# Performance work log

Hardware: AMD Instinct MI355X
Metric: run time of the kernel (lower is better)

The kernel has to match this reference:

```python
import jax, jax.numpy as jnp
import numpy as np

B, T, HID = 2, 2048, 2048
H, KVH, D = 16, 4, 128


def _rope_tables(t, d):
    inv_freq = 1.0 / (10000.0 ** (np.arange(0, d, 2, dtype=np.float32) / d))
    freqs = np.arange(t, dtype=np.float32)[:, None] * inv_freq[None, :]  # [T, d/2]
    emb = np.concatenate([freqs, freqs], axis=-1)  # [T, d]
    return jnp.asarray(np.cos(emb))[None], jnp.asarray(np.sin(emb))[None]  # [1,T,d]


def setup_inputs() -> dict:
    key = jax.random.key(0)
    ks = jax.random.split(key, 5)
    x = jax.random.normal(ks[0], (B, T, HID), dtype=jnp.float32)
    rope_cos, rope_sin = _rope_tables(T, D)
    s_in = 1.0 / np.sqrt(HID)
    Wq = jax.random.normal(ks[1], (HID, H * D), dtype=jnp.float32) * s_in
    Wk = jax.random.normal(ks[2], (HID, KVH * D), dtype=jnp.float32) * s_in
    Wv = jax.random.normal(ks[3], (HID, KVH * D), dtype=jnp.float32) * s_in
    Wo = jax.random.normal(ks[4], (H * D, HID), dtype=jnp.float32) * (1.0 / np.sqrt(H * D))
    return {"x": x, "rope_cos": rope_cos, "rope_sin": rope_sin,
            "Wq": Wq, "Wk": Wk, "Wv": Wv, "Wo": Wo}


def _apply_rope(t, cos, sin):
    # t: [B,T,h,D]; cos/sin: [1,T,D] -> broadcast over heads
    c = cos[:, :, None, :]
    s = sin[:, :, None, :]
    t1, t2 = jnp.split(t, 2, axis=-1)
    rot = jnp.concatenate([-t2, t1], axis=-1)
    return t * c + rot * s


def reference(x, rope_cos, rope_sin, Wq, Wk, Wv, Wo):
    Tq = x.shape[1]
    q = (x @ Wq).reshape(B, Tq, H, D)
    k = (x @ Wk).reshape(B, Tq, KVH, D)
    v = (x @ Wv).reshape(B, Tq, KVH, D)
    q = _apply_rope(q, rope_cos[:, :Tq], rope_sin[:, :Tq])
    k = _apply_rope(k, rope_cos[:, :Tq], rope_sin[:, :Tq])
    # sliding_window == T -> T <= W branch: k/v unchanged
    rep = H // KVH  # GQA repeat-kv
    k_full = jnp.repeat(k, rep, axis=2)  # [B,T,H,D]
    v_full = jnp.repeat(v, rep, axis=2)
    scale = 1.0 / jnp.sqrt(jnp.asarray(D, dtype=x.dtype))
    scores = jnp.einsum('bqhd,bkhd->bhqk', q, k_full) * scale
    causal = jnp.tril(jnp.ones((Tq, Tq), dtype=bool))  # end-aligned, Tk==Tq
    scores = jnp.where(causal[None, None], scores, jnp.asarray(-jnp.inf, scores.dtype))
    p = jax.nn.softmax(scores, axis=-1)
    out = jnp.einsum('bhqk,bkhd->bqhd', p, v_full)
    return out.reshape(B, Tq, H * D) @ Wo
```

## Files before the change

### kernel.cpp

```cpp
#include <hip/hip_runtime.h>
#include <hip/hip_bf16.h>

#define B_   2
#define T_   2048
#define HID_ 2048
#define H_   16
#define KVH_ 4
#define D_   128
#define GQ_  (H_ / KVH_)

#define QN_  8388608
#define KN_  2097152
#define TOTQ_ 4194304
#define TOTK_ 1048576

typedef unsigned short u16;
typedef __attribute__((ext_vector_type(8))) unsigned short us8v;
typedef __attribute__((ext_vector_type(8))) short s16x8;
typedef __attribute__((ext_vector_type(4))) float f32x4;

__device__ __forceinline__ float bf2f(u16 u) {
  return __uint_as_float(((unsigned)u) << 16);
}
__device__ __forceinline__ u16 f2bf(float f) {
  unsigned x = __float_as_uint(f);
  return (u16)((x + 0x7fffu + ((x >> 16) & 1u)) >> 16);
}

__device__ __forceinline__ void gl2lds(const void* gp, void* lp) {
  __builtin_amdgcn_global_load_lds(
      (const __attribute__((address_space(1))) unsigned int*)gp,
      (__attribute__((address_space(3))) unsigned int*)lp, 16, 0, 0);
}

__device__ __forceinline__ void probe2(const void* A, const void* W, int tid,
                                       bool* abf, bool* wbf) {
  __shared__ int cA, zA, cW, zW;
  if (tid == 0) { cA = 0; zA = 0; cW = 0; zW = 0; }
  __syncthreads();
  const int i = 16384 + tid;
  {
    const u16 raw = ((const u16*)A)[i];
    const float v = bf2f(raw);
    const bool bad = !(fabsf(v) <= 1e6f) ||
                     (v != 0.0f && fabsf(v) < 1e-10f);
    if (bad) atomicAdd(&cA, 1);
    if (((tid & 1) == 0) && raw == 0) atomicAdd(&zA, 1);
  }
  {
    const u16 raw = ((const u16*)W)[i];
    const float v = bf2f(raw);
    const bool bad = !(fabsf(v) <= 1e6f) ||
                     (v != 0.0f && fabsf(v) < 1e-10f);
    if (bad) atomicAdd(&cW, 1);
    if (((tid & 1) == 0) && raw == 0) atomicAdd(&zW, 1);
  }
  __syncthreads();
  *abf = (cA < 8) && (zA < 100);
  *wbf = (cW < 8) && (zW < 100);
}

__device__ void transp_body(const void* __restrict__ Wv_,
                            u16* __restrict__ WT, int K, int N, int bx,
                            int by, int tid) {
  bool wbf, dummy;
  probe2(Wv_, Wv_, tid, &wbf, &dummy);

  __shared__ float tile[64][65];
  const int kb = by * 64;
  const int nb = bx * 64;

  for (int it = tid; it < 512; it += 256) {
    const int r = it >> 3;
    const int g = it & 7;
    const size_t off = (size_t)(kb + r) * N + nb + g * 8;
    float f[8];
    if (wbf) {
      const us8v t8 = *(const us8v*)((const u16*)Wv_ + off);
#pragma unroll
      for (int e = 0; e < 8; ++e) f[e] = bf2f(t8[e]);
    } else {
      const float4 f0 = *(const float4*)((const float*)Wv_ + off);
      const float4 f1 = *(const float4*)((const float*)Wv_ + off + 4);
      f[0] = f0.x; f[1] = f0.y; f[2] = f0.z; f[3] = f0.w;
      f[4] = f1.x; f[5] = f1.y; f[6] = f1.z; f[7] = f1.w;
    }
#pragma unroll
    for (int e = 0; e < 8; ++e) tile[r][g * 8 + e] = f[e];
  }
  __syncthreads();
  for (int it = tid; it < 512; it += 256) {
    const int n = it >> 3;
    const int g = it & 7;
    us8v tmp;
#pragma unroll
    for (int e = 0; e < 8; ++e) tmp[e] = f2bf(tile[g * 8 + e][n]);
    *(us8v*)&WT[(size_t)(nb + n) * K + kb + g * 8] = tmp;
  }
}

__device__ void conv_body(const void* __restrict__ in, u16* __restrict__ outb,
                          int cb, int tid) {
  bool ibf, dummy;
  probe2(in, in, tid, &ibf, &dummy);
  const int idx = cb * 256 + tid;
  if (idx >= (QN_ / 8)) return;
  if (ibf) {
    *(us8v*)&outb[(size_t)idx * 8] =
        *(const us8v*)((const u16*)in + (size_t)idx * 8);
  } else {
    const float4 f0 = *(const float4*)((const float*)in + (size_t)idx * 8);
    const float4 f1 = *(const float4*)((const float*)in + (size_t)idx * 8 + 4);
    uint4 w;
    asm("v_cvt_pk_bf16_f32 %0, %1, %2" : "=v"(w.x) : "v"(f0.x), "v"(f0.y));
    asm("v_cvt_pk_bf16_f32 %0, %1, %2" : "=v"(w.y) : "v"(f0.z), "v"(f0.w));
    asm("v_cvt_pk_bf16_f32 %0, %1, %2" : "=v"(w.z) : "v"(f1.x), "v"(f1.y));
    asm("v_cvt_pk_bf16_f32 %0, %1, %2" : "=v"(w.w) : "v"(f1.z), "v"(f1.w));
    *(uint4*)&outb[(size_t)idx * 8] = w;
  }
}

__global__ __launch_bounds__(256) void prep_k(
    const void* __restrict__ Wq, const void* __restrict__ Wk,
    const void* __restrict__ Wv, const void* __restrict__ Wo,
    const void* __restrict__ x, u16* __restrict__ WqT,
    u16* __restrict__ WkT, u16* __restrict__ WvT, u16* __restrict__ WoT,
    u16* __restrict__ xb) {
  const int b = blockIdx.x;
  const int tid = threadIdx.x;
  if (b < 1024) {
    transp_body(Wq, WqT, HID_, H_ * D_, b & 31, b >> 5, tid);
  } else if (b < 1280) {
    const int bb = b - 1024;
    transp_body(Wk, WkT, HID_, KVH_ * D_, bb & 7, bb >> 3, tid);
  } else if (b < 1536) {
    const int bb = b - 1280;
    transp_body(Wv, WvT, HID_, KVH_ * D_, bb & 7, bb >> 3, tid);
  } else if (b < 2560) {
    const int bb = b - 1536;
    transp_body(Wo, WoT, H_ * D_, HID_, bb & 31, bb >> 5, tid);
  } else {
    conv_body(x, xb, b - 2560, tid);
  }
}

template <int OMODE, int BN>
__global__ __launch_bounds__(512, 4) void gemm_mfma(
    const u16* __restrict__ Ab, const u16* __restrict__ WT,
    void* __restrict__ Cv, int M, int N, int K) {
  const int tid = threadIdx.x;

  __shared__ __align__(16) u16 Alds[2][128 * 64];
  __shared__ __align__(16) u16 Blds[2][BN * 64];

  const int m0 = blockIdx.y * 128;
  const int n0 = blockIdx.x * BN;
  const int wave = tid >> 6;
  const int lane = tid & 63;
  const int wm = (wave >> 2) * 64;
  const int wn = (wave & 3) * (BN / 4);
  const int lrow = lane & 15;
  const int lq = lane >> 4;
  constexpr int NI = BN / 64;

  f32x4 acc[4][NI] = {};

#define G_STAGE64(bi, kk)                                                     \
  do {                                                                        \
    _Pragma("unroll") for (int _p = 0; _p < 2; ++_p) {                        \
      const int _it = tid + _p * 512;                                         \
      const int _r = _it >> 3, _g = _it & 7;                                  \
      const int _gs = _g ^ (_r & 7);                                          \
      gl2lds(Ab + (size_t)(m0 + _r) * K + (kk) + _gs * 8,                     \
             &Alds[bi][((tid & ~63) + _p * 512) * 8]);                        \
    }                                                                         \
    _Pragma("unroll") for (int _p = 0; _p < (BN / 64); ++_p) {                \
      const int _it = tid + _p * 512;                                         \
      const int _n = _it >> 3, _g = _it & 7;                                  \
      const int _gs = _g ^ (_n & 7);                                          \
      gl2lds(WT + (size_t)(n0 + _n) * K + (kk) + _gs * 8,                     \
             &Blds[bi][((tid & ~63) + _p * 512) * 8]);                        \
    }                                                                         \
  } while (0)

  G_STAGE64(0, 0);
  __syncthreads();

  int cur = 0;
  for (int k0 = 0; k0 < K; k0 += 64) {
    if (k0 + 64 < K) G_STAGE64(cur ^ 1, k0 + 64);

#pragma unroll
    for (int ks = 0; ks < 2; ++ks) {
      s16x8 af[4], bfr[NI];
#pragma unroll
      for (int mi = 0; mi < 4; ++mi) {
        const int row = wm + 16 * mi + lrow;
        af[mi] = *(const s16x8*)&Alds[cur][row * 64 +
                                           (((ks * 4 + lq) ^ (row & 7)) * 8)];
      }
#pragma unroll
      for (int ni = 0; ni < NI; ++ni) {
        const int row = wn + 16 * ni + lrow;
        bfr[ni] = *(const s16x8*)&Blds[cur][row * 64 +
                                            (((ks * 4 + lq) ^ (row & 7)) * 8)];
      }
      __builtin_amdgcn_s_setprio(1);
#pragma unroll
      for (int mi = 0; mi < 4; ++mi)
#pragma unroll
        for (int ni = 0; ni < NI; ++ni)
          acc[mi][ni] = __builtin_amdgcn_mfma_f32_16x16x32_bf16(
              af[mi], bfr[ni], acc[mi][ni], 0, 0, 0);
      __builtin_amdgcn_s_setprio(0);
    }

    __syncthreads();
    cur ^= 1;
  }
#undef G_STAGE64

#pragma unroll
  for (int mi = 0; mi < 4; ++mi) {
#pragma unroll
    for (int ni = 0; ni < NI; ++ni) {
      const int row0 = m0 + wm + 16 * mi + lq * 4;
      const int col = n0 + wn + 16 * ni + lrow;
#pragma unroll
      for (int r = 0; r < 4; ++r) {
        const int row = row0 + r;
        if (OMODE == 0) {
          ((float*)Cv)[(size_t)row * N + col] = acc[mi][ni][r];
        } else {
          const u16 val = f2bf(acc[mi][ni][r]);
          if (col < 2048) {
            ((u16*)Cv)[(size_t)row * 2048 + col] = val;
          } else if (col < 2560) {
            ((u16*)Cv)[QN_ + (size_t)row * 512 + (col - 2048)] = val;
          } else {
            const int c = col - 2560;
            const int kvh = c >> 7;
            const int d = c & 127;
            const int bb = row >> 11;
            const int tt = row & (T_ - 1);
            ((u16*)Cv)[QN_ + KN_ +
                       ((size_t)(bb * KVH_ + kvh) * D_ + d) * T_ + tt] = val;
          }
        }
      }
    }
  }
}

__global__ __launch_bounds__(256) void rope2(u16* __restrict__ qb,
                                             u16* __restrict__ kb,
                                             const void* __restrict__ cosT,
                                             const void* __restrict__ sinT) {
  const int tid = threadIdx.x;
  bool cbf, sbf;
  probe2(cosT, sinT, tid, &cbf, &sbf);

  int idx = blockIdx.x * 256 + tid;
  u16* t;
  int NH;
  float qs;
  if (idx < TOTQ_) {
    t = qb; NH = H_; qs = 0.08838834764831845f;
  } else {
    idx -= TOTQ_;
    if (idx >= TOTK_) return;
    t = kb; NH = KVH_; qs = 1.0f;
  }
  const int d = idx & 63;
  const int rest = idx >> 6;
  const int tt = (rest / NH) % T_;
  const size_t base = (size_t)rest * D_;
  const int ci = tt * D_ + d;
  float c1, s1, c2, s2;
  if (cbf) {
    c1 = bf2f(((const u16*)cosT)[ci]);
    c2 = bf2f(((const u16*)cosT)[ci + 64]);
  } else {
    c1 = ((const float*)cosT)[ci];
    c2 = ((const float*)cosT)[ci + 64];
  }
  if (sbf) {
    s1 = bf2f(((const u16*)sinT)[ci]);
    s2 = bf2f(((const u16*)sinT)[ci + 64]);
  } else {
    s1 = ((const float*)sinT)[ci];
    s2 = ((const float*)sinT)[ci + 64];
  }
  const float x1 = bf2f(t[base + d]);
  const float x2 = bf2f(t[base + d + 64]);
  t[base + d] = f2bf((x1 * c1 - x2 * s1) * qs);
  t[base + d + 64] = f2bf((x2 * c2 + x1 * s2) * qs);
}

#define ATT_STAGE(bi, ktile)                                                  \
  do {                                                                        \
    const int _k0 = (ktile) * 64;                                             \
    u16* _bk = &SM[(bi) * 16384];                                             \
    _Pragma("unroll") for (int _p = 0; _p < 2; ++_p) {                        \
      const int _it = tid + _p * 512;                                         \
      const int _r = _it >> 4, _s = _it & 15;                                 \
      gl2lds(kp + (size_t)(_k0 + _r) * (KVH_ * D_) + ((_s ^ (_r & 7)) * 8),   \
             &_bk[((tid & ~63) + _p * 512) * 8]);                             \
    }                                                                         \
    _Pragma("unroll") for (int _p = 0; _p < 2; ++_p) {                        \
      const int _it = tid + _p * 512;                                         \
      const int _r = _it >> 3, _s = _it & 7;                                  \
      gl2lds(vp + (size_t)_r * T_ + _k0 + ((_s ^ (_r & 7)) * 8),              \
             &_bk[8192 + ((tid & ~63) + _p * 512) * 8]);                      \
    }                                                                         \
  } while (0)

__global__ __launch_bounds__(512, 4) void attn_mfma(
    const u16* __restrict__ q, const u16* __restrict__ k,
    const u16* __restrict__ vT, u16* __restrict__ o) {
  const int tid = threadIdx.x;
  const int ip = blockIdx.y;
  const int bh = blockIdx.x;
  const int b = bh >> 4;
  const int h = bh & 15;
  const int kvh = h >> 2;
  const int hi0 = 64 * (31 - ip);
  const int lo0 = 64 * ip;

  __shared__ __align__(16) u16 SM[2 * 16384];
  __shared__ __align__(16) u16 Pl[128 * 64];

  const int wave = tid >> 6;
  const int lane = tid & 63;
  const int l15 = lane & 15;
  const int quad = lane >> 4;
  const bool isHi = wave < 4;
  const int rowbase = isHi ? (hi0 + 16 * wave) : (lo0 + 16 * (wave - 4));
  const int pr0 = 16 * wave;

  const u16* kp = k + ((size_t)b * T_ * KVH_ + kvh) * D_;
  const u16* vp = vT + (size_t)(b * KVH_ + kvh) * D_ * T_;

  s16x8 qf[4];
  {
    const size_t qrow = ((size_t)(b * T_ + rowbase + l15) * H_ + h) * D_;
#pragma unroll
    for (int st = 0; st < 4; ++st)
      qf[st] = *(const s16x8*)&q[qrow + st * 32 + quad * 8];
  }

  f32x4 acc_o[8] = {};
  float m_s = -1.0e30f, l_s = 0.0f;

  const int nkt = 32 - ip;

  ATT_STAGE(0, 0);
  __syncthreads();

  for (int kt = 0; kt < nkt; ++kt) {
    const int k0 = kt * 64;
    const u16* Ks = &SM[(kt & 1) * 16384];
    const u16* Vt = Ks + 8192;

    if (kt + 1 < nkt) ATT_STAGE((kt + 1) & 1, kt + 1);

    const bool active = isHi || (kt <= ip);
    if (active) {
      f32x4 accs[4] = {};
      __builtin_amdgcn_s_setprio(1);
#pragma unroll
      for (int st = 0; st < 4; ++st) {
        const int g = st * 4 + quad;
#pragma unroll
        for (int nt = 0; nt < 4; ++nt) {
          const int row = nt * 16 + l15;
          const s16x8 kf =
              *(const s16x8*)&Ks[row * 128 + ((g ^ (row & 7)) << 3)];
          accs[nt] = __builtin_amdgcn_mfma_f32_16x16x32_bf16(kf, qf[st],
                                                             accs[nt], 0, 0,
                                                             0);
        }
      }
      __builtin_amdgcn_s_setprio(0);

      if ((k0 + 63) > rowbase) {
        const int qg = rowbase + l15;
#pragma unroll
        for (int nt = 0; nt < 4; ++nt)
#pragma unroll
          for (int r = 0; r < 4; ++r)
            if (qg < (k0 + nt * 16 + quad * 4 + r)) accs[nt][r] = -1.0e30f;
      }

      float t0 = fmaxf(fmaxf(accs[0][0], accs[0][1]),
                       fmaxf(accs[0][2], accs[0][3]));
      float t1 = fmaxf(fmaxf(accs[1][0], accs[1][1]),
                       fmaxf(accs[1][2], accs[1][3]));
      float t2 = fmaxf(fmaxf(accs[2][0], accs[2][1]),
                       fmaxf(accs[2][2], accs[2][3]));
      float t3 = fmaxf(fmaxf(accs[3][0], accs[3][1]),
                       fmaxf(accs[3][2], accs[3][3]));
      float mx = fmaxf(fmaxf(t0, t1), fmaxf(t2, t3));
      mx = fmaxf(mx, __shfl_xor(mx, 16));
      mx = fmaxf(mx, __shfl_xor(mx, 32));

      const int defer = __all(mx <= m_s + 8.0f);
      float alv = 1.0f;
      if (!defer) {
        const float mnew = fmaxf(m_s, mx);
        alv = __expf(m_s - mnew);
        m_s = mnew;
      }

#pragma unroll
      for (int nt = 0; nt < 4; ++nt)
#pragma unroll
        for (int r = 0; r < 4; ++r)
          accs[nt][r] = __expf(accs[nt][r] - m_s);

#pragma unroll
      for (int nt = 0; nt < 4; ++nt) {
        uint2 w;
        asm("v_cvt_pk_bf16_f32 %0, %1, %2"
            : "=v"(w.x) : "v"(accs[nt][0]), "v"(accs[nt][1]));
        asm("v_cvt_pk_bf16_f32 %0, %1, %2"
            : "=v"(w.y) : "v"(accs[nt][2]), "v"(accs[nt][3]));
        const int prow = pr0 + l15;
        const int c0 = nt * 16 + quad * 4;
        *(uint2*)&Pl[prow * 64 + (((c0 >> 3) ^ (prow & 7)) << 3) + (c0 & 7)] =
            w;
      }

      float s0 = (accs[0][0] + accs[0][1]) + (accs[0][2] + accs[0][3]);
      float s1 = (accs[1][0] + accs[1][1]) + (accs[1][2] + accs[1][3]);
      float s2 = (accs[2][0] + accs[2][1]) + (accs[2][2] + accs[2][3]);
      float s3 = (accs[3][0] + accs[3][1]) + (accs[3][2] + accs[3][3]);
      float rs = (s0 + s1) + (s2 + s3);
      rs += __shfl_xor(rs, 16);
      rs += __shfl_xor(rs, 32);
      l_s = l_s * alv + rs;

      if (!defer) {
#pragma unroll
        for (int r = 0; r < 4; ++r) {
          const float a4 = __shfl(alv, 4 * quad + r);
#pragma unroll
          for (int nt2 = 0; nt2 < 8; ++nt2) acc_o[nt2][r] *= a4;
        }
      }

      asm volatile("s_waitcnt lgkmcnt(0)" ::: "memory");
      __builtin_amdgcn_sched_barrier(0);

      s16x8 pa[2];
#pragma unroll
      for (int ks = 0; ks < 2; ++ks) {
        const int row = pr0 + l15;
        const int g = ks * 4 + quad;
        pa[ks] = *(const s16x8*)&Pl[row * 64 + ((g ^ (row & 7)) << 3)];
      }
      __builtin_amdgcn_s_setprio(1);
#pragma unroll
      for (int ks = 0; ks < 2; ++ks) {
        const int g = ks * 4 + quad;
#pragma unroll
        for (int nt2 = 0; nt2 < 8; ++nt2) {
          const int row = nt2 * 16 + l15;
          const s16x8 vf =
              *(const s16x8*)&Vt[row * 64 + ((g ^ (row & 7)) << 3)];
          acc_o[nt2] = __builtin_amdgcn_mfma_f32_16x16x32_bf16(pa[ks], vf,
                                                               acc_o[nt2], 0,
                                                               0, 0);
        }
      }
      __builtin_amdgcn_s_setprio(0);
    }

    __syncthreads();
  }

  const float inv = 1.0f / l_s;
#pragma unroll
  for (int r = 0; r < 4; ++r) {
    const float linv = __shfl(inv, 4 * quad + r);
    const size_t orow =
        ((size_t)(b * T_ + rowbase + quad * 4 + r) * H_ + h) * D_;
#pragma unroll
    for (int nt2 = 0; nt2 < 8; ++nt2)
      o[orow + nt2 * 16 + l15] = f2bf(acc_o[nt2][r] * linv);
  }
}

__global__ void zero_out_k(float* __restrict__ out, int n) {
  const int i = blockIdx.x * blockDim.x + threadIdx.x;
  if (i < n) out[i] = 0.0f;
}

extern "C" void kernel_launch(void* const* d_in, const int* in_sizes, int n_in,
                              void* d_out, int out_size, void* d_ws,
                              size_t ws_size, hipStream_t stream) {
  const void* x    = d_in[0];
  const void* cosT = d_in[1];
  const void* sinT = d_in[2];
  const void* Wq   = d_in[3];
  const void* Wk   = d_in[4];
  const void* Wv   = d_in[5];
  const void* Wo   = d_in[6];
  float* out = (float*)d_out;

  const size_t QN = QN_;
  const size_t KN = KN_;
  const size_t WQT = (size_t)HID_ * (H_ * D_);
  const size_t WKT = (size_t)HID_ * (KVH_ * D_);
  const size_t need = (2 * QN + 2 * KN + 2 * WQT + 2 * WKT) * sizeof(u16);
  if (ws_size < need) {
    zero_out_k<<<(out_size + 255) / 256, 256, 0, stream>>>(out, out_size);
    return;
  }

  u16* qbuf  = (u16*)d_ws;
  u16* kbuf  = qbuf + QN;
  u16* vbufT = kbuf + KN;
  u16* obuf  = vbufT + KN;
  u16* xb    = obuf;
  u16* WqT   = obuf + QN;
  u16* WkT   = WqT + WQT;
  u16* WvT   = WkT + WKT;
  u16* WoT   = WvT + WKT;

  const int M = B_ * T_;

  prep_k<<<6656, 256, 0, stream>>>(Wq, Wk, Wv, Wo, x, WqT, WkT, WvT, WoT, xb);

  gemm_mfma<3, 192><<<dim3(3072 / 192, M / 128), dim3(512), 0, stream>>>(
      xb, WqT, qbuf, M, 3072, HID_);

  rope2<<<(TOTQ_ + TOTK_) / 256, 256, 0, stream>>>(qbuf, kbuf, cosT, sinT);

  attn_mfma<<<dim3(B_ * H_, 16), dim3(512), 0, stream>>>(
      qbuf, kbuf, vbufT, obuf);

  gemm_mfma<0, 128><<<dim3(HID_ / 128, M / 128), dim3(512), 0, stream>>>(
      obuf, WoT, out, M, HID_, H_ * D_);
}
```

Baseline: 305.4 us.

## Restructure GEMMs into 256-row tiles with 4-phase split-K LDS pipeline

Replaces the double-buffered GEMM with a kernel that uses 256-row M tiles, splits each 64-wide K step into two 32-wide halves, and interleaves global-to-LDS staging across four phases per iteration, gated by explicit vmcnt waits and barriers. Larger tiles raise MFMA work per loaded byte and the finer phase schedule is meant to hide load latency behind compute. The cost is doubled accumulator registers (occupancy hint drops from 4 to 2), fewer blocks (the QKV GEMM gets 256 blocks and the output GEMM 256), and hand-tuned waitcnt values that must match the number of loads in flight. The LDS XOR swizzle is dropped in favour of a 32-element row layout, which may change bank-conflict behaviour.

```diff
diff --git a/kernel.cpp b/kernel.cpp
--- a/kernel.cpp
+++ b/kernel.cpp
@@ -145,94 +145,133 @@
 }
 
 template <int OMODE, int BN>
-__global__ __launch_bounds__(512, 4) void gemm_mfma(
+__global__ __launch_bounds__(512, 2) void gemm_8ph(
     const u16* __restrict__ Ab, const u16* __restrict__ WT,
     void* __restrict__ Cv, int M, int N, int K) {
+  constexpr int NI = BN / 64;
+  constexpr int CPS = BN / 16;
+  constexpr int BLT = BN / 64;
+
   const int tid = threadIdx.x;
-
-  __shared__ __align__(16) u16 Alds[2][128 * 64];
-  __shared__ __align__(16) u16 Blds[2][BN * 64];
-
-  const int m0 = blockIdx.y * 128;
+  __shared__ __align__(16) u16 Alds[2][2][256 * 32];
+  __shared__ __align__(16) u16 Blds[2][2][BN * 32];
+
+  const int m0 = blockIdx.y * 256;
   const int n0 = blockIdx.x * BN;
   const int wave = tid >> 6;
   const int lane = tid & 63;
-  const int wm = (wave >> 2) * 64;
-  const int wn = (wave & 3) * (BN / 4);
-  const int lrow = lane & 15;
+  const int wm = wave >> 2;
+  const int wn = wave & 3;
+  const int l15 = lane & 15;
   const int lq = lane >> 4;
-  constexpr int NI = BN / 64;
-
-  f32x4 acc[4][NI] = {};
-
-#define G_STAGE64(bi, kk)                                                     \
-  do {                                                                        \
-    _Pragma("unroll") for (int _p = 0; _p < 2; ++_p) {                        \
-      const int _it = tid + _p * 512;                                         \
-      const int _r = _it >> 3, _g = _it & 7;                                  \
-      const int _gs = _g ^ (_r & 7);                                          \
-      gl2lds(Ab + (size_t)(m0 + _r) * K + (kk) + _gs * 8,                     \
-             &Alds[bi][((tid & ~63) + _p * 512) * 8]);                        \
-    }                                                                         \
-    _Pragma("unroll") for (int _p = 0; _p < (BN / 64); ++_p) {                \
-      const int _it = tid + _p * 512;                                         \
-      const int _n = _it >> 3, _g = _it & 7;                                  \
-      const int _gs = _g ^ (_n & 7);                                          \
-      gl2lds(WT + (size_t)(n0 + _n) * K + (kk) + _gs * 8,                     \
-             &Blds[bi][((tid & ~63) + _p * 512) * 8]);                        \
-    }                                                                         \
+
+  f32x4 acc[8][NI] = {};
+  s16x8 bfr[2][NI];
+
+  const int NT = K >> 6;
+
+  auto stageA = [&](int buf, int ks, int kk) {
+#pragma unroll
+    for (int p = 0; p < 2; ++p) {
+      const int c = wave + p * 8;
+      const int row = c * 16 + (lane >> 2);
+      const int col = (lane & 3) * 8;
+      gl2lds(Ab + (size_t)(m0 + row) * K + kk + ks * 32 + col,
+             &Alds[buf][ks][c * 512]);
+    }
+  };
+  auto stageB = [&](int buf, int kk) {
+#pragma unroll
+    for (int p = 0; p < BLT; ++p) {
+      const int c = wave + p * 8;
+      const int ks = c / CPS;
+      const int lc = c % CPS;
+      const int row = lc * 16 + (lane >> 2);
+      const int col = (lane & 3) * 8;
+      gl2lds(WT + (size_t)(n0 + row) * K + kk + ks * 32 + col,
+             &Blds[buf][ks][lc * 512]);
+    }
+  };
+
+#define VM_STEADY()                                                      \
+  do {                                                                   \
+    if constexpr (BN == 192)                                             \
+      asm volatile("s_waitcnt vmcnt(5)" ::: "memory");                   \
+    else                                                                 \
+      asm volatile("s_waitcnt vmcnt(4)" ::: "memory");                   \
   } while (0)
 
-  G_STAGE64(0, 0);
-  __syncthreads();
-
-  int cur = 0;
-  for (int k0 = 0; k0 < K; k0 += 64) {
-    if (k0 + 64 < K) G_STAGE64(cur ^ 1, k0 + 64);
-
-#pragma unroll
-    for (int ks = 0; ks < 2; ++ks) {
-      s16x8 af[4], bfr[NI];
-#pragma unroll
-      for (int mi = 0; mi < 4; ++mi) {
-        const int row = wm + 16 * mi + lrow;
-        af[mi] = *(const s16x8*)&Alds[cur][row * 64 +
-                                           (((ks * 4 + lq) ^ (row & 7)) * 8)];
-      }
-#pragma unroll
-      for (int ni = 0; ni < NI; ++ni) {
-        const int row = wn + 16 * ni + lrow;
-        bfr[ni] = *(const s16x8*)&Blds[cur][row * 64 +
-                                            (((ks * 4 + lq) ^ (row & 7)) * 8)];
-      }
-      __builtin_amdgcn_s_setprio(1);
-#pragma unroll
-      for (int mi = 0; mi < 4; ++mi)
-#pragma unroll
-        for (int ni = 0; ni < NI; ++ni)
-          acc[mi][ni] = __builtin_amdgcn_mfma_f32_16x16x32_bf16(
-              af[mi], bfr[ni], acc[mi][ni], 0, 0, 0);
-      __builtin_amdgcn_s_setprio(0);
-    }
-
-    __syncthreads();
-    cur ^= 1;
-  }
-#undef G_STAGE64
-
-#pragma unroll
-  for (int mi = 0; mi < 4; ++mi) {
+#define PHASE(ksv, hv, STAGE_STMT, END_STMT)                             \
+  {                                                                      \
+    s16x8 af[4];                                                         \
+    _Pragma("unroll") for (int mi = 0; mi < 4; ++mi)                     \
+      af[mi] = *(const s16x8*)&Alds[b][ksv][                             \
+          (wm * 128 + ((hv)*4 + mi) * 16 + l15) * 32 + lq * 8];          \
+    if ((hv) == 0) {                                                     \
+      _Pragma("unroll") for (int ni = 0; ni < NI; ++ni)                  \
+        bfr[ksv][ni] = *(const s16x8*)&Blds[b][ksv][                     \
+            (wn * (BN / 4) + ni * 16 + l15) * 32 + lq * 8];              \
+    }                                                                    \
+    STAGE_STMT;                                                          \
+    __builtin_amdgcn_sched_barrier(0);                                   \
+    __builtin_amdgcn_s_barrier();                                        \
+    asm volatile("s_waitcnt lgkmcnt(0)" ::: "memory");                   \
+    __builtin_amdgcn_sched_barrier(0);                                   \
+    __builtin_amdgcn_s_setprio(1);                                       \
+    _Pragma("unroll") for (int mi = 0; mi < 4; ++mi)                     \
+      _Pragma("unroll") for (int ni = 0; ni < NI; ++ni)                  \
+        acc[(hv)*4 + mi][ni] = __builtin_amdgcn_mfma_f32_16x16x32_bf16(  \
+            af[mi], bfr[ksv][ni], acc[(hv)*4 + mi][ni], 0, 0, 0);        \
+    __builtin_amdgcn_s_setprio(0);                                       \
+    END_STMT;                                                            \
+    __builtin_amdgcn_sched_barrier(0);                                   \
+    __builtin_amdgcn_s_barrier();                                        \
+  }
+
+  stageA(0, 0, 0);
+  stageA(0, 1, 0);
+  stageB(0, 0);
+  stageB(1, 64);
+  stageA(1, 0, 64);
+  VM_STEADY();
+  __builtin_amdgcn_sched_barrier(0);
+  __builtin_amdgcn_s_barrier();
+
+  for (int t = 0; t < NT; ++t) {
+    const int b = t & 1;
+    const int kk1 = (t + 1) << 6;
+    const int kk2 = (t + 2) << 6;
+    const bool s1 = (t + 1) < NT;
+    const bool s2 = (t + 2) < NT;
+
+    PHASE(0, 0, { if (s1) stageA(b ^ 1, 1, kk1); }, {});
+    PHASE(1, 0, {}, {});
+    PHASE(0, 1, { if (s2) stageB(b, kk2); }, {});
+    PHASE(1, 1, { if (s2) stageA(b, 0, kk2); },
+          {
+            if (s2) {
+              VM_STEADY();
+            } else if (s1) {
+              asm volatile("s_waitcnt vmcnt(0)" ::: "memory");
+            }
+          });
+  }
+#undef PHASE
+#undef VM_STEADY
+
+#pragma unroll
+  for (int mf = 0; mf < 8; ++mf) {
 #pragma unroll
     for (int ni = 0; ni < NI; ++ni) {
-      const int row0 = m0 + wm + 16 * mi + lq * 4;
-      const int col = n0 + wn + 16 * ni + lrow;
+      const int row0 = m0 + wm * 128 + mf * 16 + lq * 4;
+      const int col = n0 + wn * (BN / 4) + ni * 16 + l15;
 #pragma unroll
       for (int r = 0; r < 4; ++r) {
         const int row = row0 + r;
         if (OMODE == 0) {
-          ((float*)Cv)[(size_t)row * N + col] = acc[mi][ni][r];
+          ((float*)Cv)[(size_t)row * N + col] = acc[mf][ni][r];
         } else {
-          const u16 val = f2bf(acc[mi][ni][r]);
+          const u16 val = f2bf(acc[mf][ni][r]);
           if (col < 2048) {
             ((u16*)Cv)[(size_t)row * 2048 + col] = val;
           } else if (col < 2560) {
@@ -532,7 +571,7 @@
 
   prep_k<<<6656, 256, 0, stream>>>(Wq, Wk, Wv, Wo, x, WqT, WkT, WvT, WoT, xb);
 
-  gemm_mfma<3, 192><<<dim3(3072 / 192, M / 128), dim3(512), 0, stream>>>(
+  gemm_8ph<3, 192><<<dim3(3072 / 192, M / 256), dim3(512), 0, stream>>>(
       xb, WqT, qbuf, M, 3072, HID_);
 
   rope2<<<(TOTQ_ + TOTK_) / 256, 256, 0, stream>>>(qbuf, kbuf, cosT, sinT);
@@ -540,6 +579,6 @@
   attn_mfma<<<dim3(B_ * H_, 16), dim3(512), 0, stream>>>(
       qbuf, kbuf, vbufT, obuf);
 
-  gemm_mfma<0, 128><<<dim3(HID_ / 128, M / 128), dim3(512), 0, stream>>>(
+  gemm_8ph<0, 128><<<dim3(HID_ / 128, M / 256), dim3(512), 0, stream>>>(
       obuf, WoT, out, M, HID_, H_ * D_);
 }
```

Result: slower. 334.1 us (+9.4%).
